# Optimization experiments

Hardware: AMD Instinct MI355X
Metric: run time of the kernel (lower is better)

## Reference

```python
import jax, jax.numpy as jnp
from jax import lax
import numpy as np

B, N_VARS, M_CLAUSES, K_DIM = 1024, 64, 256, 12
MAX_ITER = 12


def setup_inputs() -> dict:
    key = jax.random.key(0)
    k1, k2, k3, k4 = jax.random.split(key, 4)
    z = jax.random.uniform(k1, (B, N_VARS), dtype=jnp.float32)          # input probabilities
    S = jax.random.normal(k2, (M_CLAUSES, N_VARS + 1), dtype=jnp.float32) * 0.2  # learnable clause matrix (col 0 = truth var)
    w = jax.random.uniform(k3, (M_CLAUSES,), dtype=jnp.float32)          # learnable clause weights
    r = jax.random.normal(k4, (B, N_VARS, K_DIM), dtype=jnp.float32)     # random init directions
    return {"z": z, "S": S, "w": w, "r": r, "max_iter": MAX_ITER}


def _mixing(z, S, w, r, max_iter):
    Bsz, n = z.shape
    m, N = S.shape  # N = n + 1 (truth variable is column 0)
    k = r.shape[-1]
    eps = jnp.float32(1e-8)

    # truth direction v_T = e_0
    vT = jnp.zeros((k,), dtype=z.dtype).at[0].set(1.0)

    # random unit directions orthogonal to v_T (zero out component along e_0)
    r_perp = r.at[..., 0].set(0.0)
    r_perp = r_perp / jnp.maximum(jnp.linalg.norm(r_perp, axis=-1, keepdims=True), eps)

    # SATNet init: v_i = -cos(pi z_i) v_T + sin(pi z_i) r_perp_i
    ang = jnp.pi * z
    Vvars = -jnp.cos(ang)[..., None] * vT + jnp.sin(ang)[..., None] * r_perp  # [B,n,k]
    V = jnp.concatenate([jnp.broadcast_to(vT, (Bsz, 1, k)), Vvars], axis=1)   # [B,N,k]

    Sw = S * w[:, None]                       # weighted clause matrix [m,N]
    W = jnp.einsum('mn,bnk->bmk', Sw, V)      # running product Sw @ V, [B,m,k]
    snrm = jnp.sum(Sw * Sw, axis=0)           # ||s_i||^2 per variable, [N]

    def coord_step(carry, i):
        V, W = carry
        s_i = Sw[:, i]                         # [m]
        v_old = V[:, i, :]                     # [B,k]
        g = jnp.einsum('bmk,m->bk', W, s_i) - snrm[i] * v_old
        v_new = -g / jnp.maximum(jnp.linalg.norm(g, axis=-1, keepdims=True), eps)
        W = W + (v_new - v_old)[:, None, :] * s_i[None, :, None]  # rank-1 update
        V = V.at[:, i, :].set(v_new)
        return (V, W), None

    def sweep(carry, _):
        carry, _ = lax.scan(coord_step, carry, jnp.arange(1, N))  # coordinate descent over variables
        return carry, None

    (V, _), _ = lax.scan(sweep, (V, W), None, length=max_iter)

    # output probabilities: z_i = arccos(-v_i . v_T) / pi
    cos = jnp.clip(-V[:, 1:, 0], -1.0 + 1e-6, 1.0 - 1e-6)
    return jnp.arccos(cos) / jnp.pi


def reference(z, S, w, r, max_iter):
    return _mixing(z, S, w, r, max_iter)
```

## Files before the change

kernel.cpp:

```cpp
#include <hip/hip_runtime.h>
#include <math.h>

#define BATCH 1024
#define NV    64
#define MC    256
#define KD    12
#define PI_F  3.14159265358979323846f

#define C0OFF  4096
#define DGAOFF 4160
#define DGBOFF 4224
#define CBUF   4288

typedef float f2  __attribute__((ext_vector_type(2)));
typedef float v4f __attribute__((ext_vector_type(4)));
typedef __attribute__((address_space(3))) float lds_f;

template <int CTRL>
__device__ __forceinline__ float dpp_addf(float x) {
  int y = __builtin_amdgcn_update_dpp(0, __float_as_int(x), CTRL, 0xF, 0xF, true);
  return x + __int_as_float(y);
}
template <int CTRL>
__device__ __forceinline__ float dpp_movf(float x) {
  return __int_as_float(
      __builtin_amdgcn_update_dpp(0, __float_as_int(x), CTRL, 0xF, 0xF, true));
}
__device__ __forceinline__ float readlane63(float x) {
  return __int_as_float(__builtin_amdgcn_readlane(__float_as_int(x), 63));
}
__device__ __forceinline__ float rlane(float x, int i) {
  return __int_as_float(__builtin_amdgcn_readlane(__float_as_int(x), i));
}

template <int IMM>
__device__ __forceinline__ void dsr(v4f& d, unsigned base) {
  asm volatile("ds_read_b128 %0, %1 offset:%2" : "=v"(d) : "v"(base), "i"(IMM));
}

__global__ void compute_C_kernel(const float* __restrict__ S,
                                 const float* __restrict__ w,
                                 float* __restrict__ Cg, int nsplit) {
  const int q = blockIdx.x;
  const int mc = blockIdx.y;
  const int j = threadIdx.x;
  if (j > NV) return;
  const int v = (q + 1) % 64 + 1;
  const int mlen = MC / nsplit;
  const int m0 = mc * mlen;
  float a0 = 0.f, a1 = 0.f, a2 = 0.f, a3 = 0.f;
  for (int m = m0; m < m0 + mlen; m += 4) {
    const float w0 = w[m], w1 = w[m + 1], w2 = w[m + 2], w3 = w[m + 3];
    a0 = fmaf(S[(m + 0) * (NV + 1) + v] * w0 * w0, S[(m + 0) * (NV + 1) + j], a0);
    a1 = fmaf(S[(m + 1) * (NV + 1) + v] * w1 * w1, S[(m + 1) * (NV + 1) + j], a1);
    a2 = fmaf(S[(m + 2) * (NV + 1) + v] * w2 * w2, S[(m + 2) * (NV + 1) + j], a2);
    a3 = fmaf(S[(m + 3) * (NV + 1) + v] * w3 * w3, S[(m + 3) * (NV + 1) + j], a3);
  }
  const float acc = (a0 + a1) + (a2 + a3);
  float* buf = Cg + mc * CBUF;
  const int p1 = (v == 1) ? 64 : (v - 1);
  const int p2 = (v == 1) ? 63 : (v == 2) ? 64 : (v - 2);
  if (j == 0) buf[C0OFF + q] = acc;
  if (j == p1) buf[DGAOFF + (v - 1)] = acc;
  if (j == p2) buf[DGBOFF + (v - 1)] = acc;
  if (j > 0) {
    const int j0 = j - 1;
    const float st = (j == v || j == p1 || j == p2) ? 0.f : acc;
    buf[q * 64 + (j0 & 3) * 16 + (j0 >> 2)] = st;
  }
}

__global__ __launch_bounds__(256, 1) void mixing_kernel(
    const float* __restrict__ z, const float* __restrict__ r,
    const float* __restrict__ Cg, const int* __restrict__ max_iter_p,
    float* __restrict__ out, int nsplit) {
  __shared__ __align__(16) float Ls[CBUF];

  const int t = threadIdx.x;
  const int l = t & 63;
  const int jg = l & 3;
  const int kk = l >> 2;
  const int b = blockIdx.x * 4 + (t >> 6);
  const int max_iter = max_iter_p[0];

  {
    const float4* src = (const float4*)Cg;
    float4* dst = (float4*)Ls;
    for (int idx = t; idx < CBUF / 4; idx += 256) {
      float4 a = src[idx];
      for (int u = 1; u < nsplit; ++u) {
        const float4 p = src[u * (CBUF / 4) + idx];
        a.x += p.x; a.y += p.y; a.z += p.z; a.w += p.w;
      }
      dst[idx] = a;
    }
  }

  const float my_e0 = (kk == 0) ? 1.f : 0.f;

  f2 Vv[8];
  #pragma unroll
  for (int p = 0; p < 8; ++p) {
    #pragma unroll
    for (int h = 0; h < 2; ++h) {
      const int j0 = jg + 8 * p + 4 * h;
      const float zv = z[b * NV + j0];
      float rp = 0.f;
      if (kk >= 1 && kk < KD) rp = r[(b * NV + j0) * KD + kk];
      float ssp = rp * rp;
      ssp += __shfl_xor(ssp, 4, 64);
      ssp += __shfl_xor(ssp, 8, 64);
      ssp += __shfl_xor(ssp, 16, 64);
      ssp += __shfl_xor(ssp, 32, 64);
      const float inv = 1.f / fmaxf(sqrtf(ssp), 1e-8f);
      const float sn = __builtin_amdgcn_sinf(0.5f * zv);
      const float cs = __builtin_amdgcn_cosf(0.5f * zv);
      const float vv = (kk == 0) ? -cs : sn * rp * inv;
      if (h) Vv[p].y = vv; else Vv[p].x = vv;
    }
  }

  __syncthreads();

  const float t0v = Ls[C0OFF + l];
  const float t1v = Ls[DGAOFF + l];
  const float t2v = Ls[DGBOFF + l];

  float P, vp1, vp2;

  {
    const int rb = 63 * 64 + jg * 16;
    const v4f c0r = *(const v4f*)&Ls[rb + 0];
    const v4f c1r = *(const v4f*)&Ls[rb + 4];
    const v4f c2r = *(const v4f*)&Ls[rb + 8];
    const v4f c3r = *(const v4f*)&Ls[rb + 12];
    f2 qa = (f2){c0r.x, c0r.y} * Vv[0];
    qa = __builtin_elementwise_fma((f2){c0r.z, c0r.w}, Vv[1], qa);
    qa = __builtin_elementwise_fma((f2){c2r.x, c2r.y}, Vv[4], qa);
    qa = __builtin_elementwise_fma((f2){c2r.z, c2r.w}, Vv[5], qa);
    f2 qb = (f2){c1r.x, c1r.y} * Vv[2];
    qb = __builtin_elementwise_fma((f2){c1r.z, c1r.w}, Vv[3], qb);
    qb = __builtin_elementwise_fma((f2){c3r.x, c3r.y}, Vv[6], qb);
    qb = __builtin_elementwise_fma((f2){c3r.z, c3r.w}, Vv[7], qb);
    const f2 qs = qa + qb;
    float q = qs.x + qs.y;
    q = dpp_addf<0xB1>(q);
    q = dpp_addf<0x4E>(q);
    q = fmaf(my_e0, Ls[C0OFF + 63], q);
    P = q;
    vp1 = dpp_movf<0xFF>(Vv[7].y);
    vp2 = dpp_movf<0xAA>(Vv[7].y);
  }

  const unsigned lbase = (unsigned)(unsigned long long)(lds_f*)&Ls[jg * 16];

  v4f Rb[16];

#define PFROW(R) \
  dsr<((((R) & 63) * 256) + 0)>(Rb[(((R) & 3) * 4) + 0], lbase); \
  dsr<((((R) & 63) * 256) + 16)>(Rb[(((R) & 3) * 4) + 1], lbase); \
  dsr<((((R) & 63) * 256) + 32)>(Rb[(((R) & 3) * 4) + 2], lbase); \
  dsr<((((R) & 63) * 256) + 48)>(Rb[(((R) & 3) * 4) + 3], lbase);

#define WAITR(SL) \
  asm volatile("s_waitcnt lgkmcnt(8)" \
               : "+v"(Rb[(SL) * 4 + 0]), "+v"(Rb[(SL) * 4 + 1]), \
                 "+v"(Rb[(SL) * 4 + 2]), "+v"(Rb[(SL) * 4 + 3]));

#define STEPF(I) { \
  constexpr int i_ = (I); \
  constexpr int j0w_ = (i_ + 63) & 63; \
  constexpr int p_ = j0w_ >> 3; \
  constexpr int h_ = (j0w_ >> 2) & 1; \
  constexpr int jgo_ = j0w_ & 3; \
  constexpr int s_ = (i_ & 3) * 4; \
   \
  WAITR(i_ & 3) \
  PFROW(i_ + 3) \
  const float da_ = rlane(t1v, i_); \
  const float db_ = rlane(t2v, i_); \
  const float c0_ = rlane(t0v, i_); \
  const float g_ = fmaf(da_, vp1, fmaf(db_, vp2, P)); \
  float t_ = g_ * g_; \
  f2 qa_ = (f2){Rb[s_ + 0].x, Rb[s_ + 0].y} * Vv[0]; \
  qa_ = __builtin_elementwise_fma((f2){Rb[s_ + 0].z, Rb[s_ + 0].w}, Vv[1], qa_); \
  t_ = dpp_addf<0x124>(t_); \
  f2 qb_ = (f2){Rb[s_ + 1].x, Rb[s_ + 1].y} * Vv[2]; \
  qb_ = __builtin_elementwise_fma((f2){Rb[s_ + 1].z, Rb[s_ + 1].w}, Vv[3], qb_); \
  t_ = dpp_addf<0x128>(t_); \
  qa_ = __builtin_elementwise_fma((f2){Rb[s_ + 2].x, Rb[s_ + 2].y}, Vv[4], qa_); \
  qa_ = __builtin_elementwise_fma((f2){Rb[s_ + 2].z, Rb[s_ + 2].w}, Vv[5], qa_); \
  t_ = dpp_addf<0x142>(t_); \
  qb_ = __builtin_elementwise_fma((f2){Rb[s_ + 3].x, Rb[s_ + 3].y}, Vv[6], qb_); \
  qb_ = __builtin_elementwise_fma((f2){Rb[s_ + 3].z, Rb[s_ + 3].w}, Vv[7], qb_); \
  t_ = dpp_addf<0x143>(t_); \
  const float n2_ = readlane63(t_); \
   \
  const f2 qs_ = qa_ + qb_; \
  float q_ = qs_.x + qs_.y; \
  q_ = dpp_addf<0xB1>(q_); \
  const float inv_ = __builtin_amdgcn_rsqf(fmaxf(n2_, 1e-16f)); \
  q_ = dpp_addf<0x4E>(q_); \
  q_ = fmaf(my_e0, c0_, q_); \
  if constexpr (h_) { Vv[p_].y = (jg == jgo_) ? vp1 : Vv[p_].y; } \
  else              { Vv[p_].x = (jg == jgo_) ? vp1 : Vv[p_].x; } \
  const float vn_ = -g_ * inv_; \
  vp2 = vp1; vp1 = vn_; P = q_; \
}

#define S4(N) STEPF((N) + 0) STEPF((N) + 1) STEPF((N) + 2) STEPF((N) + 3)
#define S16(N) S4((N) + 0) S4((N) + 4) S4((N) + 8) S4((N) + 12)

  asm volatile("s_waitcnt lgkmcnt(0)" ::: "memory");
  PFROW(0) PFROW(1) PFROW(2)

  #pragma unroll 1
  for (int it = 0; it < max_iter; ++it) {
    S16(0) S16(16) S16(32) S16(48)
  }

  Vv[7].y = (jg == 3) ? vp1 : Vv[7].y;

  __syncthreads();
  {
    float* Lw = Ls + (t >> 6) * 64;
    if (kk == 0) {
      Lw[jg +  0] = Vv[0].x; Lw[jg +  4] = Vv[0].y;
      Lw[jg +  8] = Vv[1].x; Lw[jg + 12] = Vv[1].y;
      Lw[jg + 16] = Vv[2].x; Lw[jg + 20] = Vv[2].y;
      Lw[jg + 24] = Vv[3].x; Lw[jg + 28] = Vv[3].y;
      Lw[jg + 32] = Vv[4].x; Lw[jg + 36] = Vv[4].y;
      Lw[jg + 40] = Vv[5].x; Lw[jg + 44] = Vv[5].y;
      Lw[jg + 48] = Vv[6].x; Lw[jg + 52] = Vv[6].y;
      Lw[jg + 56] = Vv[7].x; Lw[jg + 60] = Vv[7].y;
    }
    float cv = -Lw[l];
    cv = fminf(fmaxf(cv, -1.f + 1e-6f), 1.f - 1e-6f);
    out[b * NV + l] = acosf(cv) * (1.f / PI_F);
  }
}

extern "C" void kernel_launch(void* const* d_in, const int* in_sizes, int n_in,
                              void* d_out, int out_size, void* d_ws, size_t ws_size,
                              hipStream_t stream) {
  const float* z = (const float*)d_in[0];
  const float* S = (const float*)d_in[1];
  const float* w = (const float*)d_in[2];
  const float* r = (const float*)d_in[3];
  const int* max_iter = (const int*)d_in[4];
  float* Cg = (float*)d_ws;

  const int nsplit = (ws_size >= (size_t)8 * CBUF * 4) ? 8
                   : (ws_size >= (size_t)4 * CBUF * 4) ? 4 : 1;
  compute_C_kernel<<<dim3(NV, nsplit), 128, 0, stream>>>(S, w, Cg, nsplit);
  mixing_kernel<<<BATCH / 4, 256, 0, stream>>>(z, r, Cg, max_iter,
                                               (float*)d_out, nsplit);
}
```

Baseline: 141.6 us.

## Remap lanes to 8 variable groups with 2 k-components per lane

```diff
diff --git a/kernel.cpp b/kernel.cpp
--- a/kernel.cpp
+++ b/kernel.cpp
@@ -20,11 +20,6 @@
 __device__ __forceinline__ float dpp_addf(float x) {
   int y = __builtin_amdgcn_update_dpp(0, __float_as_int(x), CTRL, 0xF, 0xF, true);
   return x + __int_as_float(y);
-}
-template <int CTRL>
-__device__ __forceinline__ float dpp_movf(float x) {
-  return __int_as_float(
-      __builtin_amdgcn_update_dpp(0, __float_as_int(x), CTRL, 0xF, 0xF, true));
 }
 __device__ __forceinline__ float readlane63(float x) {
   return __int_as_float(__builtin_amdgcn_readlane(__float_as_int(x), 63));
@@ -66,7 +61,7 @@
   if (j > 0) {
     const int j0 = j - 1;
     const float st = (j == v || j == p1 || j == p2) ? 0.f : acc;
-    buf[q * 64 + (j0 & 3) * 16 + (j0 >> 2)] = st;
+    buf[q * 64 + (j0 & 7) * 8 + (j0 >> 3)] = st;
   }
 }
 
@@ -78,8 +73,8 @@
 
   const int t = threadIdx.x;
   const int l = t & 63;
-  const int jg = l & 3;
-  const int kk = l >> 2;
+  const int jgx = (l & 3) | ((l >> 1) & 4);
+  const int kl = ((l >> 2) & 1) | ((l >> 3) & 6);
   const int b = blockIdx.x * 4 + (t >> 6);
   const int max_iter = max_iter_p[0];
 
@@ -96,28 +91,26 @@
     }
   }
 
-  const float my_e0 = (kk == 0) ? 1.f : 0.f;
+  const float my_e0 = (kl == 0) ? 1.f : 0.f;
 
   f2 Vv[8];
   #pragma unroll
-  for (int p = 0; p < 8; ++p) {
-    #pragma unroll
-    for (int h = 0; h < 2; ++h) {
-      const int j0 = jg + 8 * p + 4 * h;
-      const float zv = z[b * NV + j0];
-      float rp = 0.f;
-      if (kk >= 1 && kk < KD) rp = r[(b * NV + j0) * KD + kk];
-      float ssp = rp * rp;
-      ssp += __shfl_xor(ssp, 4, 64);
-      ssp += __shfl_xor(ssp, 8, 64);
-      ssp += __shfl_xor(ssp, 16, 64);
-      ssp += __shfl_xor(ssp, 32, 64);
-      const float inv = 1.f / fmaxf(sqrtf(ssp), 1e-8f);
-      const float sn = __builtin_amdgcn_sinf(0.5f * zv);
-      const float cs = __builtin_amdgcn_cosf(0.5f * zv);
-      const float vv = (kk == 0) ? -cs : sn * rp * inv;
-      if (h) Vv[p].y = vv; else Vv[p].x = vv;
-    }
+  for (int m = 0; m < 8; ++m) {
+    const int j0 = jgx + 8 * m;
+    const float zv = z[b * NV + j0];
+    f2 rp = {0.f, 0.f};
+    if (kl < 6) rp = *(const f2*)&r[(b * NV + j0) * KD + 2 * kl];
+    if (kl == 0) rp.x = 0.f;
+    float ssp = fmaf(rp.x, rp.x, rp.y * rp.y);
+    ssp += __shfl_xor(ssp, 4, 64);
+    ssp += __shfl_xor(ssp, 16, 64);
+    ssp += __shfl_xor(ssp, 32, 64);
+    const float inv = 1.f / fmaxf(sqrtf(ssp), 1e-8f);
+    const float sn = __builtin_amdgcn_sinf(0.5f * zv);
+    const float cs = __builtin_amdgcn_cosf(0.5f * zv);
+    const float si = sn * inv;
+    Vv[m].x = (kl == 0) ? -cs : si * rp.x;
+    Vv[m].y = si * rp.y;
   }
 
   __syncthreads();
@@ -126,85 +119,80 @@
   const float t1v = Ls[DGAOFF + l];
   const float t2v = Ls[DGBOFF + l];
 
-  float P, vp1, vp2;
+  f2 P, vp1, vp2;
 
   {
-    const int rb = 63 * 64 + jg * 16;
-    const v4f c0r = *(const v4f*)&Ls[rb + 0];
-    const v4f c1r = *(const v4f*)&Ls[rb + 4];
-    const v4f c2r = *(const v4f*)&Ls[rb + 8];
-    const v4f c3r = *(const v4f*)&Ls[rb + 12];
-    f2 qa = (f2){c0r.x, c0r.y} * Vv[0];
-    qa = __builtin_elementwise_fma((f2){c0r.z, c0r.w}, Vv[1], qa);
-    qa = __builtin_elementwise_fma((f2){c2r.x, c2r.y}, Vv[4], qa);
-    qa = __builtin_elementwise_fma((f2){c2r.z, c2r.w}, Vv[5], qa);
-    f2 qb = (f2){c1r.x, c1r.y} * Vv[2];
-    qb = __builtin_elementwise_fma((f2){c1r.z, c1r.w}, Vv[3], qb);
-    qb = __builtin_elementwise_fma((f2){c3r.x, c3r.y}, Vv[6], qb);
-    qb = __builtin_elementwise_fma((f2){c3r.z, c3r.w}, Vv[7], qb);
-    const f2 qs = qa + qb;
-    float q = qs.x + qs.y;
-    q = dpp_addf<0xB1>(q);
-    q = dpp_addf<0x4E>(q);
-    q = fmaf(my_e0, Ls[C0OFF + 63], q);
+    const v4f cA = *(const v4f*)&Ls[63 * 64 + jgx * 8];
+    const v4f cB = *(const v4f*)&Ls[63 * 64 + jgx * 8 + 4];
+    f2 q = (f2){cA.x, cA.x} * Vv[0];
+    q = __builtin_elementwise_fma((f2){cA.y, cA.y}, Vv[1], q);
+    q = __builtin_elementwise_fma((f2){cA.z, cA.z}, Vv[2], q);
+    q = __builtin_elementwise_fma((f2){cA.w, cA.w}, Vv[3], q);
+    q = __builtin_elementwise_fma((f2){cB.x, cB.x}, Vv[4], q);
+    q = __builtin_elementwise_fma((f2){cB.y, cB.y}, Vv[5], q);
+    q = __builtin_elementwise_fma((f2){cB.z, cB.z}, Vv[6], q);
+    q = __builtin_elementwise_fma((f2){cB.w, cB.w}, Vv[7], q);
+    q.x = dpp_addf<0xB1>(q.x);  q.y = dpp_addf<0xB1>(q.y);
+    q.x = dpp_addf<0x4E>(q.x);  q.y = dpp_addf<0x4E>(q.y);
+    q.x = dpp_addf<0x128>(q.x); q.y = dpp_addf<0x128>(q.y);
+    q.x = fmaf(my_e0, Ls[C0OFF + 63], q.x);
     P = q;
-    vp1 = dpp_movf<0xFF>(Vv[7].y);
-    vp2 = dpp_movf<0xAA>(Vv[7].y);
-  }
-
-  const unsigned lbase = (unsigned)(unsigned long long)(lds_f*)&Ls[jg * 16];
-
-  v4f Rb[16];
+    vp1.x = __shfl(Vv[7].x, (l & 0x34) | 0x0B, 64);
+    vp1.y = __shfl(Vv[7].y, (l & 0x34) | 0x0B, 64);
+    vp2.x = __shfl(Vv[7].x, (l & 0x34) | 0x0A, 64);
+    vp2.y = __shfl(Vv[7].y, (l & 0x34) | 0x0A, 64);
+  }
+
+  const unsigned lbase = (unsigned)(unsigned long long)(lds_f*)&Ls[jgx * 8];
+
+  v4f Rb[4][2];
 
 #define PFROW(R) \
-  dsr<((((R) & 63) * 256) + 0)>(Rb[(((R) & 3) * 4) + 0], lbase); \
-  dsr<((((R) & 63) * 256) + 16)>(Rb[(((R) & 3) * 4) + 1], lbase); \
-  dsr<((((R) & 63) * 256) + 32)>(Rb[(((R) & 3) * 4) + 2], lbase); \
-  dsr<((((R) & 63) * 256) + 48)>(Rb[(((R) & 3) * 4) + 3], lbase);
+  dsr<((((R) & 63) * 256) + 0)>(Rb[(R) & 3][0], lbase); \
+  dsr<((((R) & 63) * 256) + 16)>(Rb[(R) & 3][1], lbase);
 
 #define WAITR(SL) \
-  asm volatile("s_waitcnt lgkmcnt(8)" \
-               : "+v"(Rb[(SL) * 4 + 0]), "+v"(Rb[(SL) * 4 + 1]), \
-                 "+v"(Rb[(SL) * 4 + 2]), "+v"(Rb[(SL) * 4 + 3]));
+  asm volatile("s_waitcnt lgkmcnt(4)" : "+v"(Rb[SL][0]), "+v"(Rb[SL][1]));
 
 #define STEPF(I) { \
   constexpr int i_ = (I); \
+  constexpr int s_ = i_ & 3; \
   constexpr int j0w_ = (i_ + 63) & 63; \
-  constexpr int p_ = j0w_ >> 3; \
-  constexpr int h_ = (j0w_ >> 2) & 1; \
-  constexpr int jgo_ = j0w_ & 3; \
-  constexpr int s_ = (i_ & 3) * 4; \
-   \
-  WAITR(i_ & 3) \
+  constexpr int m_ = j0w_ >> 3; \
+  constexpr int jgo_ = j0w_ & 7; \
+  WAITR(s_) \
   PFROW(i_ + 3) \
   const float da_ = rlane(t1v, i_); \
   const float db_ = rlane(t2v, i_); \
   const float c0_ = rlane(t0v, i_); \
-  const float g_ = fmaf(da_, vp1, fmaf(db_, vp2, P)); \
-  float t_ = g_ * g_; \
-  f2 qa_ = (f2){Rb[s_ + 0].x, Rb[s_ + 0].y} * Vv[0]; \
-  qa_ = __builtin_elementwise_fma((f2){Rb[s_ + 0].z, Rb[s_ + 0].w}, Vv[1], qa_); \
-  t_ = dpp_addf<0x124>(t_); \
-  f2 qb_ = (f2){Rb[s_ + 1].x, Rb[s_ + 1].y} * Vv[2]; \
-  qb_ = __builtin_elementwise_fma((f2){Rb[s_ + 1].z, Rb[s_ + 1].w}, Vv[3], qb_); \
-  t_ = dpp_addf<0x128>(t_); \
-  qa_ = __builtin_elementwise_fma((f2){Rb[s_ + 2].x, Rb[s_ + 2].y}, Vv[4], qa_); \
-  qa_ = __builtin_elementwise_fma((f2){Rb[s_ + 2].z, Rb[s_ + 2].w}, Vv[5], qa_); \
-  t_ = dpp_addf<0x142>(t_); \
-  qb_ = __builtin_elementwise_fma((f2){Rb[s_ + 3].x, Rb[s_ + 3].y}, Vv[6], qb_); \
-  qb_ = __builtin_elementwise_fma((f2){Rb[s_ + 3].z, Rb[s_ + 3].w}, Vv[7], qb_); \
-  t_ = dpp_addf<0x143>(t_); \
+   \
+  f2 g_; \
+  g_.x = fmaf(da_, vp1.x, fmaf(db_, vp2.x, P.x)); \
+  g_.y = fmaf(da_, vp1.y, fmaf(db_, vp2.y, P.y)); \
+  float t_ = fmaf(g_.x, g_.x, g_.y * g_.y); \
+  const v4f ceA = Rb[s_][0], ceB = Rb[s_][1]; \
+  f2 q_ = (f2){ceA.x, ceA.x} * Vv[0]; \
+  q_ = __builtin_elementwise_fma((f2){ceA.y, ceA.y}, Vv[1], q_); \
+  t_ = dpp_addf<0x124>(t_);             \
+  q_ = __builtin_elementwise_fma((f2){ceA.z, ceA.z}, Vv[2], q_); \
+  q_ = __builtin_elementwise_fma((f2){ceA.w, ceA.w}, Vv[3], q_); \
+  t_ = dpp_addf<0x142>(t_);             \
+  q_ = __builtin_elementwise_fma((f2){ceB.x, ceB.x}, Vv[4], q_); \
+  q_ = __builtin_elementwise_fma((f2){ceB.y, ceB.y}, Vv[5], q_); \
+  t_ = dpp_addf<0x143>(t_);             \
+  q_ = __builtin_elementwise_fma((f2){ceB.z, ceB.z}, Vv[6], q_); \
+  q_ = __builtin_elementwise_fma((f2){ceB.w, ceB.w}, Vv[7], q_); \
   const float n2_ = readlane63(t_); \
+  const float inv_ = __builtin_amdgcn_rsqf(fmaxf(n2_, 1e-16f)); \
+  q_.x = dpp_addf<0xB1>(q_.x);  q_.y = dpp_addf<0xB1>(q_.y); \
+  f2 vn_; vn_.x = -g_.x * inv_; vn_.y = -g_.y * inv_; \
+  q_.x = dpp_addf<0x4E>(q_.x);  q_.y = dpp_addf<0x4E>(q_.y); \
+  q_.x = dpp_addf<0x128>(q_.x); q_.y = dpp_addf<0x128>(q_.y); \
+  q_.x = fmaf(my_e0, c0_, q_.x); \
    \
-  const f2 qs_ = qa_ + qb_; \
-  float q_ = qs_.x + qs_.y; \
-  q_ = dpp_addf<0xB1>(q_); \
-  const float inv_ = __builtin_amdgcn_rsqf(fmaxf(n2_, 1e-16f)); \
-  q_ = dpp_addf<0x4E>(q_); \
-  q_ = fmaf(my_e0, c0_, q_); \
-  if constexpr (h_) { Vv[p_].y = (jg == jgo_) ? vp1 : Vv[p_].y; } \
-  else              { Vv[p_].x = (jg == jgo_) ? vp1 : Vv[p_].x; } \
-  const float vn_ = -g_ * inv_; \
+  Vv[m_].x = (jgx == jgo_) ? vp1.x : Vv[m_].x; \
+  Vv[m_].y = (jgx == jgo_) ? vp1.y : Vv[m_].y; \
+   \
   vp2 = vp1; vp1 = vn_; P = q_; \
 }
 
@@ -219,21 +207,18 @@
     S16(0) S16(16) S16(32) S16(48)
   }
 
-  Vv[7].y = (jg == 3) ? vp1 : Vv[7].y;
-
+  Vv[7].x = (jgx == 7) ? vp1.x : Vv[7].x;
+  Vv[7].y = (jgx == 7) ? vp1.y : Vv[7].y;
+
+  asm volatile("s_waitcnt lgkmcnt(0)" ::: "memory");
   __syncthreads();
   {
     float* Lw = Ls + (t >> 6) * 64;
-    if (kk == 0) {
-      Lw[jg +  0] = Vv[0].x; Lw[jg +  4] = Vv[0].y;
-      Lw[jg +  8] = Vv[1].x; Lw[jg + 12] = Vv[1].y;
-      Lw[jg + 16] = Vv[2].x; Lw[jg + 20] = Vv[2].y;
-      Lw[jg + 24] = Vv[3].x; Lw[jg + 28] = Vv[3].y;
-      Lw[jg + 32] = Vv[4].x; Lw[jg + 36] = Vv[4].y;
-      Lw[jg + 40] = Vv[5].x; Lw[jg + 44] = Vv[5].y;
-      Lw[jg + 48] = Vv[6].x; Lw[jg + 52] = Vv[6].y;
-      Lw[jg + 56] = Vv[7].x; Lw[jg + 60] = Vv[7].y;
+    if (kl == 0) {
+      #pragma unroll
+      for (int m = 0; m < 8; ++m) Lw[jgx + 8 * m] = Vv[m].x;
     }
+    __builtin_amdgcn_s_waitcnt(0);
     float cv = -Lw[l];
     cv = fminf(fmaxf(cv, -1.f + 1e-6f), 1.f - 1e-6f);
     out[b * NV + l] = acosf(cv) * (1.f / PI_F);
```

New measurement: 141.7 us. No clear change (+0.1%).
